# Performance work log

Measured on AMD Instinct MI355X. Metric: run time of the kernel, lower is better.

## Reference

```python
import jax, jax.numpy as jnp
import numpy as np
from jax import lax

B, S, C = 32, 4096, 512   # batch, seq_len, input_dim
P, K = 3, 10              # pairs_per_fan_in, max_fan_in


def setup_inputs() -> dict:
    key = jax.random.key(0)
    keys = jax.random.split(key, K + 1)
    inp = {"x": jax.random.normal(keys[0], (B, S, C), dtype=jnp.float32)}
    for k in range(1, K + 1):
        # WIO layout: (kernel_width=k, in_channels=C, out_channels=P)
        fan_in = C * k
        scale = 1.0 / np.sqrt(fan_in)  # kaiming-uniform-ish scale
        inp[f"w{k}"] = scale * jax.random.normal(keys[k], (k, C, P), dtype=jnp.float32)
    return inp


def _causal_conv(x, w):
    # x: (B, S, C), w: (k, C, P) -> (B, S, P); left-pad k-1 == torch padding=k-1 then [:, :, :S]
    k = w.shape[0]
    return lax.conv_general_dilated(
        x, w, window_strides=(1,), padding=[(k - 1, 0)],
        dimension_numbers=("NWC", "WIO", "NWC"))


def reference(x, w1, w2, w3, w4, w5, w6, w7, w8, w9, w10) -> jnp.ndarray:
    ws = (w1, w2, w3, w4, w5, w6, w7, w8, w9, w10)
    # ReLU each causal conv output, concat along feature dim -> (B, S, K*P)
    parts = [jax.nn.relu(_causal_conv(x, w)) for w in ws]
    return jnp.concatenate(parts, axis=-1)
```

## Files before the change

kernel.cpp:

```cpp
#include <hip/hip_runtime.h>

typedef __attribute__((ext_vector_type(8))) short short8;
typedef __attribute__((ext_vector_type(4))) float f32x4;

#define C_DIM 512
#define S_DIM 4096
#define NCOL 165
#define NCOLP 176
#define LDK 32
#define M_TILE 80
#define M_OUT 64
#define BK 32
#define NCHUNK 16

__device__ __forceinline__ unsigned short f2bf(float f) {
  unsigned u = __builtin_bit_cast(unsigned, f);
  u += 0x7fffu + ((u >> 16) & 1u);
  return (unsigned short)(u >> 16);
}
__device__ __forceinline__ float bf2f(unsigned short h) {
  unsigned u = ((unsigned)h) << 16;
  return __builtin_bit_cast(float, u);
}

struct WP { const float* w[10]; };

__global__ __launch_bounds__(256) void prep_kernel(WP wp, unsigned short* bt_hi,
                                                   unsigned short* bt_lo) {
  int idx = blockIdx.x * 256 + threadIdx.x;
  int col = idx >> 9;
  int c = idx & 511;
  float v = 0.f;
  if (col < NCOL) {
    int kw = 1, base = 0;
    while (col >= base + 3 * kw) { base += 3 * kw; ++kw; }
    int rem = col - base;
    int t = rem / 3, p = rem - 3 * t;
    v = wp.w[kw - 1][(t * C_DIM + c) * 3 + p];
  }
  unsigned short hi = f2bf(v);
  unsigned short lo = f2bf(v - bf2f(hi));
  bt_hi[col * C_DIM + c] = hi;
  bt_lo[col * C_DIM + c] = lo;
}

__device__ __forceinline__ void gld16(const void* g, void* l) {
  __builtin_amdgcn_global_load_lds(
      (const __attribute__((address_space(1))) unsigned int*)(const unsigned int*)g,
      (__attribute__((address_space(3))) unsigned int*)(unsigned int*)l, 16, 0, 0);
}

__device__ __forceinline__ void cvt_pack(const float4 v, uint2& hi, uint2& lo) {
  unsigned u0 = __builtin_bit_cast(unsigned, v.x);
  unsigned u1 = __builtin_bit_cast(unsigned, v.y);
  unsigned u2 = __builtin_bit_cast(unsigned, v.z);
  unsigned u3 = __builtin_bit_cast(unsigned, v.w);
  unsigned r0 = u0 + 0x7fffu + ((u0 >> 16) & 1u);
  unsigned r1 = u1 + 0x7fffu + ((u1 >> 16) & 1u);
  unsigned r2 = u2 + 0x7fffu + ((u2 >> 16) & 1u);
  unsigned r3 = u3 + 0x7fffu + ((u3 >> 16) & 1u);
  hi.x = __builtin_amdgcn_perm(r1, r0, 0x07060302u);
  hi.y = __builtin_amdgcn_perm(r3, r2, 0x07060302u);
  float m0 = v.x - __builtin_bit_cast(float, r0 & 0xffff0000u);
  float m1 = v.y - __builtin_bit_cast(float, r1 & 0xffff0000u);
  float m2 = v.z - __builtin_bit_cast(float, r2 & 0xffff0000u);
  float m3 = v.w - __builtin_bit_cast(float, r3 & 0xffff0000u);
  unsigned w0 = __builtin_bit_cast(unsigned, m0); w0 += 0x7fffu + ((w0 >> 16) & 1u);
  unsigned w1 = __builtin_bit_cast(unsigned, m1); w1 += 0x7fffu + ((w1 >> 16) & 1u);
  unsigned w2 = __builtin_bit_cast(unsigned, m2); w2 += 0x7fffu + ((w2 >> 16) & 1u);
  unsigned w3 = __builtin_bit_cast(unsigned, m3); w3 += 0x7fffu + ((w3 >> 16) & 1u);
  lo.x = __builtin_amdgcn_perm(w1, w0, 0x07060302u);
  lo.y = __builtin_amdgcn_perm(w3, w2, 0x07060302u);
}

__global__ __launch_bounds__(256, 4) void conv_kernel(const float* __restrict__ x,
                                                      const unsigned short* __restrict__ bt_hi,
                                                      const unsigned short* __restrict__ bt_lo,
                                                      float* __restrict__ out) {
  __shared__ __align__(16) unsigned char smem[32768];
  unsigned short* As_hi = (unsigned short*)smem;
  unsigned short* As_lo = (unsigned short*)(smem + 5120);
  unsigned short* Bs_hi = (unsigned short*)(smem + 10240);
  unsigned short* Bs_lo = (unsigned short*)(smem + 21504);
  float* Ys = (float*)smem;

  const int tid = threadIdx.x;
  const int b = blockIdx.x >> 6;
  const int tile = blockIdx.x & 63;
  const int s0 = tile * M_OUT;
  const int sBase = s0 - 16;
  const int wave = tid >> 6;
  const int lane = tid & 63;
  const int lane15 = lane & 15;
  const int quad = lane >> 4;
  const int n0 = wave * 3;
  const int nmine = (wave < 3) ? 3 : 2;

  const float4* aptr[3];
  bool aexists[3], avalid[3];
  int arow[3], aq[3];
#pragma unroll
  for (int i = 0; i < 3; ++i) {
    int idx = tid + i * 256;
    aexists[i] = (idx < 640);
    arow[i] = idx >> 3;
    aq[i] = idx & 7;
    int s = sBase + arow[i];
    avalid[i] = aexists[i] && (s >= 0);
    aptr[i] = (const float4*)&x[((size_t)(b * S_DIM + (s < 0 ? 0 : s))) * C_DIM + aq[i] * 4];
  }

  float4 pf[3];
  f32x4 acc[5][3];
#pragma unroll
  for (int m = 0; m < 5; ++m)
#pragma unroll
    for (int n = 0; n < 3; ++n) acc[m][n] = (f32x4){0.f, 0.f, 0.f, 0.f};

  auto loadA = [&](int ch) {
#pragma unroll
    for (int i = 0; i < 3; ++i) {
      if (avalid[i]) pf[i] = aptr[i][ch * 8];
      else pf[i] = make_float4(0.f, 0.f, 0.f, 0.f);
    }
  };
  auto cvtWrite = [&]() {
#pragma unroll
    for (int i = 0; i < 3; ++i) {
      if (aexists[i]) {
        uint2 hi, lo;
        cvt_pack(pf[i], hi, lo);
        *(uint2*)&As_hi[arow[i] * LDK + aq[i] * 4] = hi;
        *(uint2*)&As_lo[arow[i] * LDK + aq[i] * 4] = lo;
      }
    }
  };
  auto dmaB = [&](int ch) {
    const int kc = ch * BK;
    for (int j = wave; j < 22; j += 4) {
      int jj = (j < 11) ? j : j - 11;
      const unsigned short* src = (j < 11) ? bt_hi : bt_lo;
      unsigned short* dst = (j < 11) ? Bs_hi : Bs_lo;
      int col = jj * 16 + (lane >> 2);
      int part = lane & 3;
      gld16(src + col * C_DIM + kc + part * 8, dst + jj * 512);
    }
  };

  loadA(0);
  cvtWrite();
  dmaB(0);
  __syncthreads();

  for (int ch = 0; ch < NCHUNK; ++ch) {
    if (ch < NCHUNK - 1) loadA(ch + 1);

    short8 bh[3], bl[3];
#pragma unroll
    for (int nn = 0; nn < 3; ++nn) {
      if (nn < nmine) {
        int cr = (n0 + nn) * 16 + lane15;
        bh[nn] = *(const short8*)&Bs_hi[cr * LDK + quad * 8];
        bl[nn] = *(const short8*)&Bs_lo[cr * LDK + quad * 8];
      }
    }
#pragma unroll
    for (int m = 0; m < 5; ++m) {
      int ar = m * 16 + lane15;
      short8 ah = *(const short8*)&As_hi[ar * LDK + quad * 8];
      short8 al = *(const short8*)&As_lo[ar * LDK + quad * 8];
#pragma unroll
      for (int nn = 0; nn < 3; ++nn) {
        if (nn < nmine) {
          acc[m][nn] = __builtin_amdgcn_mfma_f32_16x16x32_bf16(ah, bh[nn], acc[m][nn], 0, 0, 0);
          acc[m][nn] = __builtin_amdgcn_mfma_f32_16x16x32_bf16(ah, bl[nn], acc[m][nn], 0, 0, 0);
          acc[m][nn] = __builtin_amdgcn_mfma_f32_16x16x32_bf16(al, bh[nn], acc[m][nn], 0, 0, 0);
        }
      }
    }
    __syncthreads();
    if (ch < NCHUNK - 1) {
      cvtWrite();
      dmaB(ch + 1);
      __syncthreads();
    }
  }

#pragma unroll
  for (int i = 1; i <= 4; ++i) {
    if (i == 1) {
#pragma unroll
      for (int nn = 0; nn < 3; ++nn)
        if (nn < nmine)
#pragma unroll
          for (int r = 0; r < 4; ++r)
            Ys[0 * 2816 + (quad * 4 + r) * NCOLP + (n0 + nn) * 16 + lane15] = acc[0][nn][r];
    }
#pragma unroll
    for (int nn = 0; nn < 3; ++nn)
      if (nn < nmine)
#pragma unroll
        for (int r = 0; r < 4; ++r)
          Ys[(i & 1) * 2816 + (quad * 4 + r) * NCOLP + (n0 + nn) * 16 + lane15] = acc[i][nn][r];
    __syncthreads();
    for (int o = tid; o < 480; o += 256) {
      int r = o / 30;
      int j = o - 30 * r;
      int kw = j / 3 + 1;
      int p = j - (kw - 1) * 3;
      int base = 3 * (kw * (kw - 1)) / 2;
      float sum = 0.f;
      for (int d = 0; d < kw; ++d) {
        int rr = r - d;
        int slot = (rr >= 0) ? (i & 1) : ((i ^ 1) & 1);
        int lr = (rr >= 0) ? rr : (16 + rr);
        int colv = base + (kw - 1 - d) * 3 + p;
        sum += Ys[slot * 2816 + lr * NCOLP + colv];
      }
      int s = s0 + 16 * (i - 1) + r;
      out[((size_t)(b * S_DIM + s)) * 30 + j] = fmaxf(sum, 0.f);
    }
    __syncthreads();
  }
}

extern "C" void kernel_launch(void* const* d_in, const int* in_sizes, int n_in,
                              void* d_out, int out_size, void* d_ws, size_t ws_size,
                              hipStream_t stream) {
  const float* x = (const float*)d_in[0];
  WP wp;
  for (int k = 0; k < 10; ++k) wp.w[k] = (const float*)d_in[k + 1];
  unsigned short* bt_hi = (unsigned short*)d_ws;
  unsigned short* bt_lo = bt_hi + NCOLP * C_DIM;
  prep_kernel<<<NCOLP * C_DIM / 256, 256, 0, stream>>>(wp, bt_hi, bt_lo);
  conv_kernel<<<32 * (S_DIM / M_OUT), 256, 0, stream>>>(x, bt_hi, bt_lo, (float*)d_out);
}
```

Before: 412.8 us.

## Double-buffer A tile in LDS, read B fragments directly from global

Switches the A tile in shared memory to a double buffer with a prefetch two chunks ahead. The main loop now has one barrier per chunk instead of two. The B-weight tiles are no longer staged into LDS with DMA; each wave loads its MFMA B fragments straight from global memory, relying on cache reuse. The LDS row strides are padded (LDK 40, Ys stride 180) to reduce bank conflicts. The risk is extra global and L2 traffic for B, plus load latency on the MFMA critical path.

Result: slower. 439.8 us (+6.5%).

```diff
diff --git a/kernel.cpp b/kernel.cpp
--- a/kernel.cpp
+++ b/kernel.cpp
@@ -7,11 +7,12 @@
 #define S_DIM 4096
 #define NCOL 165
 #define NCOLP 176
-#define LDK 32
-#define M_TILE 80
+#define LDK 40
 #define M_OUT 64
 #define BK 32
 #define NCHUNK 16
+#define YST 180
+#define YSLOT 2880
 
 __device__ __forceinline__ unsigned short f2bf(float f) {
   unsigned u = __builtin_bit_cast(unsigned, f);
@@ -42,12 +43,6 @@
   unsigned short lo = f2bf(v - bf2f(hi));
   bt_hi[col * C_DIM + c] = hi;
   bt_lo[col * C_DIM + c] = lo;
-}
-
-__device__ __forceinline__ void gld16(const void* g, void* l) {
-  __builtin_amdgcn_global_load_lds(
-      (const __attribute__((address_space(1))) unsigned int*)(const unsigned int*)g,
-      (__attribute__((address_space(3))) unsigned int*)(unsigned int*)l, 16, 0, 0);
 }
 
 __device__ __forceinline__ void cvt_pack(const float4 v, uint2& hi, uint2& lo) {
@@ -77,11 +72,7 @@
                                                       const unsigned short* __restrict__ bt_hi,
                                                       const unsigned short* __restrict__ bt_lo,
                                                       float* __restrict__ out) {
-  __shared__ __align__(16) unsigned char smem[32768];
-  unsigned short* As_hi = (unsigned short*)smem;
-  unsigned short* As_lo = (unsigned short*)(smem + 5120);
-  unsigned short* Bs_hi = (unsigned short*)(smem + 10240);
-  unsigned short* Bs_lo = (unsigned short*)(smem + 21504);
+  __shared__ __align__(16) unsigned char smem[25600];
   float* Ys = (float*)smem;
 
   const int tid = threadIdx.x;
@@ -96,6 +87,20 @@
   const int n0 = wave * 3;
   const int nmine = (wave < 3) ? 3 : 2;
 
+  const short8* bph[3];
+  const short8* bpl[3];
+#pragma unroll
+  for (int nn = 0; nn < 3; ++nn) {
+    int cr = (n0 + nn) * 16 + lane15;
+    if (nn < nmine) {
+      bph[nn] = (const short8*)&bt_hi[cr * C_DIM + quad * 8];
+      bpl[nn] = (const short8*)&bt_lo[cr * C_DIM + quad * 8];
+    } else {
+      bph[nn] = (const short8*)&bt_hi[quad * 8];
+      bpl[nn] = (const short8*)&bt_lo[quad * 8];
+    }
+  }
+
   const float4* aptr[3];
   bool aexists[3], avalid[3];
   int arow[3], aq[3];
@@ -124,51 +129,41 @@
       else pf[i] = make_float4(0.f, 0.f, 0.f, 0.f);
     }
   };
-  auto cvtWrite = [&]() {
+  auto cvtWrite = [&](int buf) {
+    unsigned short* Ah = (unsigned short*)(smem + buf * 12800);
+    unsigned short* Al = (unsigned short*)(smem + buf * 12800 + 6400);
 #pragma unroll
     for (int i = 0; i < 3; ++i) {
       if (aexists[i]) {
         uint2 hi, lo;
         cvt_pack(pf[i], hi, lo);
-        *(uint2*)&As_hi[arow[i] * LDK + aq[i] * 4] = hi;
-        *(uint2*)&As_lo[arow[i] * LDK + aq[i] * 4] = lo;
+        *(uint2*)&Ah[arow[i] * LDK + aq[i] * 4] = hi;
+        *(uint2*)&Al[arow[i] * LDK + aq[i] * 4] = lo;
       }
     }
   };
-  auto dmaB = [&](int ch) {
-    const int kc = ch * BK;
-    for (int j = wave; j < 22; j += 4) {
-      int jj = (j < 11) ? j : j - 11;
-      const unsigned short* src = (j < 11) ? bt_hi : bt_lo;
-      unsigned short* dst = (j < 11) ? Bs_hi : Bs_lo;
-      int col = jj * 16 + (lane >> 2);
-      int part = lane & 3;
-      gld16(src + col * C_DIM + kc + part * 8, dst + jj * 512);
-    }
-  };
 
   loadA(0);
-  cvtWrite();
-  dmaB(0);
+  cvtWrite(0);
+  loadA(1);
   __syncthreads();
 
   for (int ch = 0; ch < NCHUNK; ++ch) {
-    if (ch < NCHUNK - 1) loadA(ch + 1);
-
+    const unsigned short* Ah = (const unsigned short*)(smem + (ch & 1) * 12800);
+    const unsigned short* Al = (const unsigned short*)(smem + (ch & 1) * 12800 + 6400);
     short8 bh[3], bl[3];
 #pragma unroll
     for (int nn = 0; nn < 3; ++nn) {
       if (nn < nmine) {
-        int cr = (n0 + nn) * 16 + lane15;
-        bh[nn] = *(const short8*)&Bs_hi[cr * LDK + quad * 8];
-        bl[nn] = *(const short8*)&Bs_lo[cr * LDK + quad * 8];
+        bh[nn] = bph[nn][ch * 4];
+        bl[nn] = bpl[nn][ch * 4];
       }
     }
 #pragma unroll
     for (int m = 0; m < 5; ++m) {
       int ar = m * 16 + lane15;
-      short8 ah = *(const short8*)&As_hi[ar * LDK + quad * 8];
-      short8 al = *(const short8*)&As_lo[ar * LDK + quad * 8];
+      short8 ah = *(const short8*)&Ah[ar * LDK + quad * 8];
+      short8 al = *(const short8*)&Al[ar * LDK + quad * 8];
 #pragma unroll
       for (int nn = 0; nn < 3; ++nn) {
         if (nn < nmine) {
@@ -178,12 +173,11 @@
         }
       }
     }
+    if (ch < NCHUNK - 1) {
+      cvtWrite((ch + 1) & 1);
+      if (ch < NCHUNK - 2) loadA(ch + 2);
+    }
     __syncthreads();
-    if (ch < NCHUNK - 1) {
-      cvtWrite();
-      dmaB(ch + 1);
-      __syncthreads();
-    }
   }
 
 #pragma unroll
@@ -194,14 +188,14 @@
         if (nn < nmine)
 #pragma unroll
           for (int r = 0; r < 4; ++r)
-            Ys[0 * 2816 + (quad * 4 + r) * NCOLP + (n0 + nn) * 16 + lane15] = acc[0][nn][r];
+            Ys[0 * YSLOT + (quad * 4 + r) * YST + (n0 + nn) * 16 + lane15] = acc[0][nn][r];
     }
 #pragma unroll
     for (int nn = 0; nn < 3; ++nn)
       if (nn < nmine)
 #pragma unroll
         for (int r = 0; r < 4; ++r)
-          Ys[(i & 1) * 2816 + (quad * 4 + r) * NCOLP + (n0 + nn) * 16 + lane15] = acc[i][nn][r];
+          Ys[(i & 1) * YSLOT + (quad * 4 + r) * YST + (n0 + nn) * 16 + lane15] = acc[i][nn][r];
     __syncthreads();
     for (int o = tid; o < 480; o += 256) {
       int r = o / 30;
@@ -215,7 +209,7 @@
         int slot = (rr >= 0) ? (i & 1) : ((i ^ 1) & 1);
         int lr = (rr >= 0) ? rr : (16 + rr);
         int colv = base + (kw - 1 - d) * 3 + p;
-        sum += Ys[slot * 2816 + lr * NCOLP + colv];
+        sum += Ys[slot * YSLOT + lr * YST + colv];
       }
       int s = s0 + 16 * (i - 1) + r;
       out[((size_t)(b * S_DIM + s)) * 30 + j] = fmaxf(sum, 0.f);
```
